# Optimization experiments

Measured on AMD Instinct MI355X. Metric: run time of the kernel, lower is better.

## Reference

```python
import jax, jax.numpy as jnp
import numpy as np

R = 32  # voxel resolution
B, CIN, COUT, N = 4, 64, 64, 4096
K = 3


def setup_inputs():
    key = jax.random.key(0)
    ks = jax.random.split(key, 8)
    s = 0.05
    return {
        "features": jax.random.normal(ks[0], (B, CIN, N), jnp.float32),
        "coords": jax.random.normal(ks[1], (B, 3, N), jnp.float32),
        # voxel branch: conv3d + BN x2
        "w1": jax.random.normal(ks[2], (COUT, CIN, K, K, K), jnp.float32) * s,
        "b1": jnp.zeros((COUT,), jnp.float32),
        "g1": jnp.ones((COUT,), jnp.float32),
        "be1": jnp.zeros((COUT,), jnp.float32),
        "w2": jax.random.normal(ks[3], (COUT, COUT, K, K, K), jnp.float32) * s,
        "b2": jnp.zeros((COUT,), jnp.float32),
        "g2": jnp.ones((COUT,), jnp.float32),
        "be2": jnp.zeros((COUT,), jnp.float32),
        # point branch SharedMLP (1x1 conv + BN + ReLU)
        "wp": jax.random.normal(ks[4], (COUT, CIN), jnp.float32) * s,
        "bp": jnp.zeros((COUT,), jnp.float32),
        "gp": jnp.ones((COUT,), jnp.float32),
        "bep": jnp.zeros((COUT,), jnp.float32),
        # fuzzy_proj 1x1 conv
        "wf": jax.random.normal(ks[5], (COUT, CIN), jnp.float32) * s,
        "bf": jnp.zeros((COUT,), jnp.float32),
        # fusion SharedMLP (3*COUT -> COUT)
        "wfu": jax.random.normal(ks[6], (COUT, 3 * COUT), jnp.float32) * s,
        "bfu": jnp.zeros((COUT,), jnp.float32),
        "gfu": jnp.ones((COUT,), jnp.float32),
        "befu": jnp.zeros((COUT,), jnp.float32),
    }


def _bn3d(x, g, b):
    # training-mode BatchNorm3d, eps=1e-4 (biased variance, as torch)
    m = x.mean((0, 2, 3, 4), keepdims=True)
    v = x.var((0, 2, 3, 4), keepdims=True)
    return (x - m) * jax.lax.rsqrt(v + 1e-4) * g[None, :, None, None, None] + b[None, :, None, None, None]


def _bn1d(x, g, b):
    m = x.mean((0, 2), keepdims=True)
    v = x.var((0, 2), keepdims=True)
    return (x - m) * jax.lax.rsqrt(v + 1e-4) * g[None, :, None] + b[None, :, None]


def _conv3d(x, w, b):
    pad = K // 2
    y = jax.lax.conv_general_dilated(x, w, (1, 1, 1), [(pad, pad)] * 3,
                                     dimension_numbers=('NCDHW', 'OIDHW', 'NCDHW'))
    return y + b[None, :, None, None, None]


def _conv1x1(x, w, b):
    return jnp.einsum('oc,bcn->bon', w, x) + b[None, :, None]


def _voxelize(features, coords):
    # PVCNN Voxelization(normalize=True, eps=0): center, scale to unit, grid coords in [0, R-1]
    nc = coords - coords.mean(axis=2, keepdims=True)              # [B,3,N]
    norm = jnp.linalg.norm(nc, axis=1, keepdims=True)             # [B,1,N]
    nc = nc / (norm.max(axis=2, keepdims=True) * 2.0) + 0.5
    nc = jnp.clip(nc * R, 0.0, R - 1)
    vox = jnp.round(nc).astype(jnp.int32)                         # [B,3,N]
    b_, c_, n_ = features.shape
    idx = (vox[:, 0] * R + vox[:, 1]) * R + vox[:, 2]             # [B,N]
    flat = (idx + jnp.arange(b_)[:, None] * R ** 3).reshape(-1)
    feat = features.transpose(0, 2, 1).reshape(b_ * n_, c_)
    sums = jax.ops.segment_sum(feat, flat, num_segments=b_ * R ** 3)
    cnt = jax.ops.segment_sum(jnp.ones((b_ * n_,), feat.dtype), flat, num_segments=b_ * R ** 3)
    avg = sums / jnp.maximum(cnt, 1.0)[:, None]                   # scatter-mean
    grid = avg.reshape(b_, R ** 3, c_).transpose(0, 2, 1).reshape(b_, c_, R, R, R)
    return grid, nc


def _devoxelize(grid, nc):
    # trilinear gather: grid [B,C,R,R,R], nc [B,3,N] float coords in [0,R-1]
    b_, c_ = grid.shape[:2]
    g = grid.reshape(b_, c_, -1)
    lo_f = jnp.floor(nc)
    fr = nc - lo_f                                                # fractional part [B,3,N]
    lo = lo_f.astype(jnp.int32)
    hi = jnp.minimum(lo + 1, R - 1)
    out = jnp.zeros((b_, c_, nc.shape[2]), grid.dtype)
    for dx in (0, 1):
        for dy in (0, 1):
            for dz in (0, 1):
                ix = hi[:, 0] if dx else lo[:, 0]
                iy = hi[:, 1] if dy else lo[:, 1]
                iz = hi[:, 2] if dz else lo[:, 2]
                w = ((fr[:, 0] if dx else 1.0 - fr[:, 0]) *
                     (fr[:, 1] if dy else 1.0 - fr[:, 1]) *
                     (fr[:, 2] if dz else 1.0 - fr[:, 2]))        # [B,N]
                flat = (ix * R + iy) * R + iz                     # [B,N]
                vals = jnp.take_along_axis(g, flat[:, None, :], axis=2)  # [B,C,N]
                out = out + vals * w[:, None, :]
    return out


def reference(features, coords, w1, b1, g1, be1, w2, b2, g2, be2,
              wp, bp, gp, bep, wf, bf, wfu, bfu, gfu, befu):
    lrelu = lambda x: jnp.where(x > 0, x, 0.1 * x)
    # voxel branch
    grid, nc = _voxelize(features, coords)
    v = lrelu(_bn3d(_conv3d(grid, w1, b1), g1, be1))
    v = lrelu(_bn3d(_conv3d(v, w2, b2), g2, be2))
    vox_feat = _devoxelize(v, nc)                                 # [B,COUT,N]
    # point branch
    pt = jax.nn.relu(_bn1d(_conv1x1(features, wp, bp), gp, bep))
    # fuzzy branch: dense attention over points
    cn = coords.transpose(0, 2, 1)                                # [B,N,3]
    cn = cn / jnp.maximum(jnp.linalg.norm(cn, axis=-1, keepdims=True), 1e-12)
    att = jax.nn.softmax(jnp.einsum('bnd,bmd->bnm', cn, cn) / 0.1, axis=-1)
    fz = jnp.einsum('bnm,bcm->bcn', att, features)                # [B,CIN,N]
    fz = _conv1x1(fz, wf, bf)
    # fusion
    comb = jnp.concatenate([vox_feat, pt, fz], axis=1)            # [B,3*COUT,N]
    fused = jax.nn.relu(_bn1d(_conv1x1(comb, wfu, bfu), gfu, befu))
    return (fused, coords)
```

## Files before the change

### kernel.cpp

```cpp
#include <hip/hip_runtime.h>
#include <hip/hip_bf16.h>
#include <math.h>

#define RR 32
#define R3 32768
#define BB 4
#define CI 64
#define CO 64
#define NN 4096

typedef short v8s __attribute__((ext_vector_type(8)));
typedef float v4f __attribute__((ext_vector_type(4)));
typedef unsigned short ushort_t;

__device__ __forceinline__ unsigned short f2bf(float f) {
    unsigned int u = __float_as_uint(f);
    unsigned int r = (u + 0x7FFFu + ((u >> 16) & 1u)) >> 16;
    return (unsigned short)r;
}

__device__ __forceinline__ void gll16(const void* g, void* l) {
    __builtin_amdgcn_global_load_lds((const __attribute__((address_space(1))) unsigned int*)g,
                                     (__attribute__((address_space(3))) unsigned int*)l, 16, 0, 0);
}

__device__ __forceinline__ float blockReduceSum(float v, float* sm) {
    int tid = threadIdx.x;
    sm[tid] = v; __syncthreads();
    for (int off = 128; off > 0; off >>= 1) {
        if (tid < off) sm[tid] += sm[tid + off];
        __syncthreads();
    }
    float r = sm[0]; __syncthreads();
    return r;
}
__device__ __forceinline__ float blockReduceMax(float v, float* sm) {
    int tid = threadIdx.x;
    sm[tid] = v; __syncthreads();
    for (int off = 128; off > 0; off >>= 1) {
        if (tid < off) sm[tid] = fmaxf(sm[tid], sm[tid + off]);
        __syncthreads();
    }
    float r = sm[0]; __syncthreads();
    return r;
}

__global__ void k_nc(const float* __restrict__ coords, float* __restrict__ nc,
                     int* __restrict__ vidx, int* __restrict__ cntI) {
    int b = blockIdx.x, tid = threadIdx.x;
    __shared__ float sm[256];
    const float* cb = coords + (size_t)b * 3 * NN;
    float s0 = 0, s1 = 0, s2 = 0;
    for (int n = tid; n < NN; n += 256) {
        s0 += cb[n]; s1 += cb[NN + n]; s2 += cb[2 * NN + n];
    }
    float m0 = blockReduceSum(s0, sm) * (1.0f / NN);
    float m1 = blockReduceSum(s1, sm) * (1.0f / NN);
    float m2 = blockReduceSum(s2, sm) * (1.0f / NN);
    float mx = 0;
    for (int n = tid; n < NN; n += 256) {
        float dx = cb[n] - m0, dy = cb[NN + n] - m1, dz = cb[2 * NN + n] - m2;
        mx = fmaxf(mx, dx * dx + dy * dy + dz * dz);
    }
    mx = blockReduceMax(mx, sm);
    float denom = 2.0f * sqrtf(mx);
    float mean[3] = {m0, m1, m2};
    for (int n = tid; n < NN; n += 256) {
        int vi[3];
        #pragma unroll
        for (int ax = 0; ax < 3; ax++) {
            float x = (cb[ax * NN + n] - mean[ax]) / denom + 0.5f;
            x = x * RR;
            x = fminf(fmaxf(x, 0.0f), (float)(RR - 1));
            nc[((size_t)b * 3 + ax) * NN + n] = x;
            vi[ax] = (int)rintf(x);
        }
        int idx = (vi[0] * RR + vi[1]) * RR + vi[2];
        vidx[b * NN + n] = idx;
        atomicAdd(&cntI[b * R3 + idx], 1);
    }
}

__global__ void k_scan1(const int* __restrict__ cntI, int* __restrict__ lscan,
                        int* __restrict__ bsum) {
    __shared__ int sm[256];
    int tid = threadIdx.x;
    int i = blockIdx.x * 256 + tid;
    int v = cntI[i];
    sm[tid] = v; __syncthreads();
    for (int off = 1; off < 256; off <<= 1) {
        int t = (tid >= off) ? sm[tid - off] : 0;
        __syncthreads();
        sm[tid] += t;
        __syncthreads();
    }
    lscan[i] = sm[tid] - v;
    if (tid == 255) bsum[blockIdx.x] = sm[tid];
}

__global__ void k_scan2(const int* __restrict__ bsum, int* __restrict__ bbase) {
    __shared__ int sm[512];
    int tid = threadIdx.x;
    int v = bsum[tid];
    sm[tid] = v; __syncthreads();
    for (int off = 1; off < 512; off <<= 1) {
        int t = (tid >= off) ? sm[tid - off] : 0;
        __syncthreads();
        sm[tid] += t;
        __syncthreads();
    }
    bbase[tid] = sm[tid] - v;
}

__global__ void k_fill(const int* __restrict__ vidx, const int* __restrict__ lscan,
                       const int* __restrict__ bbase, int* __restrict__ rank,
                       int* __restrict__ plist) {
    int i = blockIdx.x * 256 + threadIdx.x;
    int b = i >> 12, n = i & (NN - 1);
    int flat = b * R3 + vidx[i];
    int r = atomicAdd(&rank[flat], 1);
    plist[bbase[flat >> 8] + lscan[flat] + r] = n;
}

__global__ void k_tfcl(const float* __restrict__ feat, float* __restrict__ featT) {
    __shared__ float t[64][65];
    int b = blockIdx.y, n0 = blockIdx.x * 64, tid = threadIdx.x;
    int q = tid >> 6, nl = tid & 63;
    #pragma unroll
    for (int k = 0; k < 16; k++) {
        int c = q * 16 + k;
        t[nl][c] = feat[((size_t)(b * CI + c)) * NN + n0 + nl];
    }
    __syncthreads();
    #pragma unroll
    for (int k = 0; k < 16; k++) {
        int n = q * 16 + k;
        featT[((size_t)b * NN + n0 + n) * 64 + nl] = t[n][nl];
    }
}

__global__ __launch_bounds__(256) void k_gather(const float* __restrict__ featT,
                                                const int* __restrict__ cntI,
                                                const int* __restrict__ lscan,
                                                const int* __restrict__ bbase,
                                                const int* __restrict__ plist,
                                                ushort_t* __restrict__ gT) {
    int wv = threadIdx.x >> 6, lane = threadIdx.x & 63;
    int vbase = blockIdx.x * 32 + wv * 8;
    for (int k = 0; k < 8; k++) {
        int flat = vbase + k;
        int count = cntI[flat];
        float s = 0.0f;
        if (count > 0) {
            int b = flat >> 15;
            int start = bbase[flat >> 8] + lscan[flat];
            for (int j = 0; j < count; j++) {
                int n = plist[start + j];
                s += featT[((size_t)b * NN + n) * 64 + lane];
            }
            s *= 1.0f / (float)count;
        }
        gT[(size_t)flat * 64 + lane] = f2bf(s);
    }
}

__global__ void k_f2b(const float* __restrict__ x, ushort_t* __restrict__ o) {
    size_t i = (size_t)blockIdx.x * 256 + threadIdx.x;
    float4 a = ((const float4*)x)[i * 2];
    float4 b = ((const float4*)x)[i * 2 + 1];
    union { __hip_bfloat162 h[4]; uint4 u; } pk;
    pk.h[0] = __float22bfloat162_rn(make_float2(a.x, a.y));
    pk.h[1] = __float22bfloat162_rn(make_float2(a.z, a.w));
    pk.h[2] = __float22bfloat162_rn(make_float2(b.x, b.y));
    pk.h[3] = __float22bfloat162_rn(make_float2(b.z, b.w));
    ((uint4*)o)[i] = pk.u;
}

__global__ void k_tws(const float* __restrict__ w, ushort_t* __restrict__ wS) {
    int i = blockIdx.x * 256 + threadIdx.x;
    int cis = i & 31, co = (i >> 5) & 63;
    int dx = (i >> 11) % 3, cih = (i / 6144) & 1, dzdy = i / 12288;
    int k = dzdy * 3 + dx, ci = cih * 32 + cis;
    wS[i] = f2bf(w[((size_t)co * CI + ci) * 27 + k]);
}

__global__ void k_fold(const float* __restrict__ wp, const float* __restrict__ wfu,
                       const float* __restrict__ wf, const float* __restrict__ bf,
                       const float* __restrict__ bfu,
                       float* __restrict__ wpT, float* __restrict__ wfuT,
                       float* __restrict__ bC) {
    int i = blockIdx.x * 256 + threadIdx.x;
    if (i < 4096) {
        int c = i >> 6, o = i & 63;
        wpT[c * 64 + o] = wp[o * 64 + c];
    } else if (i < 12288) {
        int j = i - 4096;
        int c = j >> 6, o = j & 63;
        wfuT[c * 64 + o] = wfu[(size_t)o * 192 + c];
    } else if (i < 16384) {
        int j = i - 12288;
        int c = j >> 6, o = j & 63;
        float s = 0;
        for (int k = 0; k < 64; k++)
            s += wfu[(size_t)o * 192 + 128 + k] * wf[(size_t)k * 64 + c];
        wfuT[(128 + c) * 64 + o] = s;
    } else if (i < 16448) {
        int o = i - 16384;
        float s = bfu[o];
        for (int k = 0; k < 64; k++)
            s += wfu[(size_t)o * 192 + 128 + k] * bf[k];
        bC[o] = s;
    }
}

__global__ void k_bncast(const float* __restrict__ x, const float* __restrict__ accs,
                         const float* __restrict__ g, const float* __restrict__ be,
                         float invcnt, float slope, ushort_t* __restrict__ o) {
    size_t i = (size_t)blockIdx.x * 256 + threadIdx.x;
    int c0 = (int)((i * 8) & 63);
    float sc[8], sh[8];
    #pragma unroll
    for (int j = 0; j < 8; j++) {
        int c = c0 + j;
        float mean = accs[2 * c] * invcnt;
        float var = accs[2 * c + 1] * invcnt - mean * mean;
        float scale = g[c] * rsqrtf(var + 1e-4f);
        sc[j] = scale;
        sh[j] = be[c] - mean * scale;
    }
    float4 a = ((const float4*)x)[i * 2];
    float4 d = ((const float4*)x)[i * 2 + 1];
    float va[8] = {a.x, a.y, a.z, a.w, d.x, d.y, d.z, d.w};
    unsigned pk[4];
    #pragma unroll
    for (int j = 0; j < 4; j++) {
        float u0 = va[2 * j] * sc[2 * j] + sh[2 * j];
        float u1 = va[2 * j + 1] * sc[2 * j + 1] + sh[2 * j + 1];
        u0 = u0 > 0 ? u0 : slope * u0;
        u1 = u1 > 0 ? u1 : slope * u1;
        pk[j] = (unsigned)f2bf(u0) | ((unsigned)f2bf(u1) << 16);
    }
    ((uint4*)o)[i] = make_uint4(pk[0], pk[1], pk[2], pk[3]);
}

__global__ __launch_bounds__(256) void k_convlds(const ushort_t* __restrict__ gT,
                                                 const ushort_t* __restrict__ wS,
                                                 float* __restrict__ outCL,
                                                 float* __restrict__ accs) {
    __shared__ ushort_t lin[20480];
    __shared__ ushort_t lw[2][6144];
    int bid = blockIdx.x;
    int wgid = (bid & 7) * 64 + (bid >> 3);
    int yt = wgid & 3, z0 = (wgid >> 2) & 31, b = wgid >> 7;
    int tid = threadIdx.x;
    int w = __builtin_amdgcn_readfirstlane(tid >> 6);
    int lane = tid & 63, l15 = lane & 15, l4 = lane >> 4;
    int y0 = yt * 8;
    const ushort_t* gTb = gT + (size_t)b * R3 * 64;

    int voxF[4];
    #pragma unroll
    for (int f = 0; f < 4; f++)
        voxF[f] = (w * 2 + (f >> 1)) * 32 + (f & 1) * 16 + l15 - 1;
    bool xlo_ok = (l15 != 0), xhi_ok = (l15 != 15);

    const v8s vzero = {};
    v4f acc[4][4];
    #pragma unroll
    for (int m = 0; m < 4; m++)
        #pragma unroll
        for (int f = 0; f < 4; f++)
            acc[m][f] = (v4f){0.0f, 0.0f, 0.0f, 0.0f};

#define WSTAGE(s)                                                              \
    do {                                                                       \
        const ushort_t* _src = wS + (size_t)(s) * 6144;                        \
        ushort_t* _dst = lw[(s) & 1];                                          \
        _Pragma("unroll") for (int _i = 0; _i < 3; _i++) {                     \
            int _p = _i * 256 + w * 64;                                        \
            gll16(_src + (size_t)(_p + lane) * 8, _dst + (size_t)_p * 8);      \
        }                                                                      \
    } while (0)

#define ISTAGE(dz)                                                             \
    do {                                                                       \
        int _zp = z0 - 1 + (dz);                                               \
        if (_zp < 0 || _zp > 31) {                                             \
            for (int _q = 0; _q < 10; _q++)                                    \
                *(v8s*)&lin[(size_t)(w * 640 + _q * 64 + lane) * 8] = vzero;   \
        } else {                                                               \
            if (yt == 0) *(v8s*)&lin[(size_t)tid * 8] = vzero;                 \
            if (yt == 3) *(v8s*)&lin[(size_t)(2304 + tid) * 8] = vzero;        \
            const ushort_t* _pb = gTb + ((size_t)_zp * 1024 + (size_t)(y0 - 1) * 32) * 64; \
            int _g0 = (yt == 0) ? 256 : 0;                                     \
            int _nc = 10 - (yt == 0) - (yt == 3);                              \
            for (int _i = 0; _i < _nc; _i++) {                                 \
                int _pbase = _g0 + _i * 256 + w * 64;                          \
                int _p = _pbase + lane;                                        \
                int _vx = _p >> 3, _js = _p & 7;                               \
                int _sg = _vx * 8 + (_js ^ (_vx & 7));                         \
                gll16(_pb + (size_t)_sg * 8, lin + (size_t)_pbase * 8);        \
            }                                                                  \
        }                                                                      \
    } while (0)

    WSTAGE(0);
    for (int s = 0; s < 18; s++) {
        int dy = (s / 2) % 3, cih = s & 1;
        asm volatile("s_barrier" ::: "memory");
        if ((s % 6) == 0) ISTAGE(s / 6);
        if (s + 1 < 18) WSTAGE(s + 1);
        if (s + 1 < 18) asm volatile("s_waitcnt vmcnt(3) lgkmcnt(0)" ::: "memory");
        else            asm volatile("s_waitcnt vmcnt(0) lgkmcnt(0)" ::: "memory");
        asm volatile("s_barrier" ::: "memory");

        const ushort_t* lwb = lw[s & 1];
        #pragma unroll
        for (int dx = 0; dx < 3; dx++) {
            v8s Bf[4];
            #pragma unroll
            for (int f = 0; f < 4; f++) {
                int vox = voxF[f] + dy * 32 + dx;
                int g = vox * 8 + ((cih * 4 + l4) ^ (vox & 7));
                int bix = g * 16;
                bix = bix < 0 ? 0 : bix;
                v8s vb = *(const v8s*)((const char*)lin + bix);
                bool ok = (dx == 0 && (f & 1) == 0) ? xlo_ok :
                          (dx == 2 && (f & 1) == 1) ? xhi_ok : true;
                Bf[f] = ok ? vb : vzero;
            }
            const ushort_t* ap = lwb + dx * 2048 + l15 * 32 + l4 * 8;
            #pragma unroll
            for (int m = 0; m < 4; m++) {
                v8s Af = *(const v8s*)(ap + m * 512);
                #pragma unroll
                for (int f = 0; f < 4; f++)
                    acc[m][f] = __builtin_amdgcn_mfma_f32_16x16x32_bf16(Af, Bf[f], acc[m][f], 0, 0, 0);
            }
        }
    }

    #pragma unroll
    for (int m = 0; m < 4; m++) {
        #pragma unroll
        for (int f = 0; f < 4; f++) {
            int y = y0 + w * 2 + (f >> 1);
            int x = (f & 1) * 16 + l15;
            float4 o = make_float4(acc[m][f][0], acc[m][f][1], acc[m][f][2], acc[m][f][3]);
            *(float4*)&outCL[((size_t)b * R3 + z0 * 1024 + y * 32 + x) * 64 + m * 16 + l4 * 4] = o;
        }
    }

    __syncthreads();
    float* sbuf = (float*)lin;
    #pragma unroll
    for (int m = 0; m < 4; m++)
        #pragma unroll
        for (int r = 0; r < 4; r++) {
            float s = 0, q = 0;
            #pragma unroll
            for (int f = 0; f < 4; f++) {
                float v = acc[m][f][r];
                s += v; q += v * v;
            }
            sbuf[tid * 32 + (m * 4 + r) * 2] = s;
            sbuf[tid * 32 + (m * 4 + r) * 2 + 1] = q;
        }
    __syncthreads();
    if (tid < 128) {
        int co = tid >> 1, val = tid & 1;
        int m = co >> 4, cl4 = (co >> 2) & 3, r = co & 3;
        float a = 0;
        for (int w2 = 0; w2 < 4; w2++)
            for (int l = 0; l < 16; l++)
                a += sbuf[(w2 * 64 + cl4 * 16 + l) * 32 + (m * 4 + r) * 2 + val];
        atomicAdd(&accs[2 * co + val], a);
    }
#undef WSTAGE
#undef ISTAGE
}

__global__ void k_bnfin2(const float* __restrict__ pst, const float* __restrict__ g,
                         const float* __restrict__ be, float* __restrict__ stats,
                         float invcnt) {
    int c = blockIdx.x, tid = threadIdx.x;
    __shared__ float rs[256], rq[256];
    rs[tid] = pst[(c * 256 + tid) * 2];
    rq[tid] = pst[(c * 256 + tid) * 2 + 1];
    __syncthreads();
    for (int off = 128; off > 0; off >>= 1) {
        if (tid < off) { rs[tid] += rs[tid + off]; rq[tid] += rq[tid + off]; }
        __syncthreads();
    }
    if (tid == 0) {
        float mean = rs[0] * invcnt;
        float var = rq[0] * invcnt - mean * mean;
        float sc = g[c] * rsqrtf(var + 1e-4f);
        stats[2 * c] = sc;
        stats[2 * c + 1] = be[c] - mean * sc;
    }
}

__global__ void k_bn_act(const float* __restrict__ x, const float* __restrict__ stats,
                         float* __restrict__ out, int shift, float slope) {
    size_t i = (size_t)blockIdx.x * 256 + threadIdx.x;
    int c = (int)((i >> shift) & 63);
    float sc = stats[2 * c], sh = stats[2 * c + 1];
    float4 v = ((const float4*)x)[i];
    v.x = v.x * sc + sh; v.y = v.y * sc + sh; v.z = v.z * sc + sh; v.w = v.w * sc + sh;
    v.x = v.x > 0 ? v.x : slope * v.x;
    v.y = v.y > 0 ? v.y : slope * v.y;
    v.z = v.z > 0 ? v.z : slope * v.z;
    v.w = v.w > 0 ? v.w : slope * v.w;
    ((float4*)out)[i] = v;
}

__global__ void k_devox2(const float* __restrict__ gcl, const float* __restrict__ accs,
                         const float* __restrict__ g, const float* __restrict__ be,
                         float invcnt, const float* __restrict__ nc,
                         float* __restrict__ out) {
    int b = blockIdx.y;
    int tid = threadIdx.x, p = tid >> 4, q = tid & 15;
    int n = blockIdx.x * 16 + p;
    float x = nc[((size_t)b * 3 + 0) * NN + n];
    float y = nc[((size_t)b * 3 + 1) * NN + n];
    float z = nc[((size_t)b * 3 + 2) * NN + n];
    float fx = floorf(x), fy = floorf(y), fz = floorf(z);
    int lx = (int)fx, ly = (int)fy, lz = (int)fz;
    int hx = min(lx + 1, RR - 1), hy = min(ly + 1, RR - 1), hz = min(lz + 1, RR - 1);
    float frx = x - fx, fry = y - fy, frz = z - fz;
    int xx[2] = {lx, hx}, yy[2] = {ly, hy}, zz[2] = {lz, hz};
    float wx[2] = {1.0f - frx, frx}, wy[2] = {1.0f - fry, fry}, wz[2] = {1.0f - frz, frz};
    float sc[4], sh[4];
    #pragma unroll
    for (int j = 0; j < 4; j++) {
        int c = q * 4 + j;
        float mean = accs[2 * c] * invcnt;
        float var = accs[2 * c + 1] * invcnt - mean * mean;
        float scale = g[c] * rsqrtf(var + 1e-4f);
        sc[j] = scale;
        sh[j] = be[c] - mean * scale;
    }
    float a0 = 0, a1 = 0, a2 = 0, a3 = 0;
    #pragma unroll
    for (int dx = 0; dx < 2; dx++)
        #pragma unroll
        for (int dy = 0; dy < 2; dy++)
            #pragma unroll
            for (int dz = 0; dz < 2; dz++) {
                int idx = (xx[dx] * RR + yy[dy]) * RR + zz[dz];
                float wt = wx[dx] * wy[dy] * wz[dz];
                float4 v = *(const float4*)&gcl[((size_t)b * R3 + idx) * 64 + q * 4];
                float u0 = v.x * sc[0] + sh[0]; u0 = u0 > 0 ? u0 : 0.1f * u0;
                float u1 = v.y * sc[1] + sh[1]; u1 = u1 > 0 ? u1 : 0.1f * u1;
                float u2 = v.z * sc[2] + sh[2]; u2 = u2 > 0 ? u2 : 0.1f * u2;
                float u3 = v.w * sc[3] + sh[3]; u3 = u3 > 0 ? u3 : 0.1f * u3;
                a0 += wt * u0; a1 += wt * u1; a2 += wt * u2; a3 += wt * u3;
            }
    out[((size_t)(b * 64 + q * 4 + 0)) * NN + n] = a0;
    out[((size_t)(b * 64 + q * 4 + 1)) * NN + n] = a1;
    out[((size_t)(b * 64 + q * 4 + 2)) * NN + n] = a2;
    out[((size_t)(b * 64 + q * 4 + 3)) * NN + n] = a3;
}

__global__ __launch_bounds__(256) void k_fuzzym(const float* __restrict__ coords,
                                                const ushort_t* __restrict__ featb,
                                                float* __restrict__ pnum,
                                                float* __restrict__ pden) {
    __shared__ float cm[3][1024];
    __shared__ ushort_t la[2][2048];
    int b = blockIdx.z, mc = blockIdx.y, nt = blockIdx.x;
    int tid = threadIdx.x;
    int w = tid >> 6, lane = tid & 63, l15 = lane & 15, l4 = lane >> 4;
    int m0 = mc * 1024;

    for (int i = tid; i < 1024; i += 256) {
        float a0 = coords[((size_t)b * 3 + 0) * NN + m0 + i];
        float a1 = coords[((size_t)b * 3 + 1) * NN + m0 + i];
        float a2 = coords[((size_t)b * 3 + 2) * NN + m0 + i];
        float inv = 1.0f / fmaxf(sqrtf(a0 * a0 + a1 * a1 + a2 * a2), 1e-12f);
        cm[0][i] = a0 * inv; cm[1][i] = a1 * inv; cm[2][i] = a2 * inv;
    }

    int n = nt * 64 + w * 16 + l15;
    float q0 = coords[((size_t)b * 3 + 0) * NN + n];
    float q1 = coords[((size_t)b * 3 + 1) * NN + n];
    float q2 = coords[((size_t)b * 3 + 2) * NN + n];
    float qi = 10.0f / fmaxf(sqrtf(q0 * q0 + q1 * q1 + q2 * q2), 1e-12f);
    q0 *= qi; q1 *= qi; q2 *= qi;

    int srow = tid >> 2, sslot = tid & 3;
    int g0 = sslot ^ ((srow >> 1) & 3);
    const ushort_t* fb = featb + (size_t)b * 64 * NN + m0;
    const ushort_t* sbase = fb + (size_t)srow * NN + g0 * 8;
    int rsw = (l15 >> 1) & 3;

    v4f acc[4];
    #pragma unroll
    for (int cb = 0; cb < 4; cb++) acc[cb] = (v4f){0.0f, 0.0f, 0.0f, 0.0f};
    float den = 0.0f;

    gll16(sbase, &la[0][(size_t)tid * 8]);
    asm volatile("s_waitcnt vmcnt(0)" ::: "memory");
    __syncthreads();

    for (int t = 0; t < 32; t++) {
        int cur = t & 1;
        if (t + 1 < 32)
            gll16(sbase + (t + 1) * 32, &la[cur ^ 1][(size_t)tid * 8]);

        int mo = t * 32 + l4 * 8;
        float e[8];
        #pragma unroll
        for (int jj = 0; jj < 2; jj++) {
            float4 x0 = *(const float4*)&cm[0][mo + jj * 4];
            float4 x1 = *(const float4*)&cm[1][mo + jj * 4];
            float4 x2 = *(const float4*)&cm[2][mo + jj * 4];
            e[jj * 4 + 0] = __expf(q0 * x0.x + q1 * x1.x + q2 * x2.x);
            e[jj * 4 + 1] = __expf(q0 * x0.y + q1 * x1.y + q2 * x2.y);
            e[jj * 4 + 2] = __expf(q0 * x0.z + q1 * x1.z + q2 * x2.z);
            e[jj * 4 + 3] = __expf(q0 * x0.w + q1 * x1.w + q2 * x2.w);
        }
        den += ((e[0] + e[1]) + (e[2] + e[3])) + ((e[4] + e[5]) + (e[6] + e[7]));
        union { __hip_bfloat162 h[4]; v8s v; } pk;
        pk.h[0] = __float22bfloat162_rn(make_float2(e[0], e[1]));
        pk.h[1] = __float22bfloat162_rn(make_float2(e[2], e[3]));
        pk.h[2] = __float22bfloat162_rn(make_float2(e[4], e[5]));
        pk.h[3] = __float22bfloat162_rn(make_float2(e[6], e[7]));
        #pragma unroll
        for (int cb = 0; cb < 4; cb++) {
            v8s A = *(const v8s*)&la[cur][(size_t)((cb * 16 + l15) * 4 + (l4 ^ rsw)) * 8];
            acc[cb] = __builtin_amdgcn_mfma_f32_16x16x32_bf16(A, pk.v, acc[cb], 0, 0, 0);
        }
        asm volatile("s_waitcnt vmcnt(0)" ::: "memory");
        __syncthreads();
    }

    den += __shfl_xor(den, 16);
    den += __shfl_xor(den, 32);

    size_t obase = ((size_t)(b * 4 + mc)) * 64 * NN;
    #pragma unroll
    for (int cb = 0; cb < 4; cb++)
        #pragma unroll
        for (int r = 0; r < 4; r++)
            pnum[obase + (size_t)(cb * 16 + l4 * 4 + r) * NN + n] = acc[cb][r];
    if (l4 == 0) pden[((size_t)(b * 4 + mc)) * NN + n] = den;
}

__global__ void k_combine2(const float* __restrict__ pnum, const float* __restrict__ pden,
                           float* __restrict__ fzf) {
    int i = blockIdx.x * 256 + threadIdx.x;
    int b = i >> 18, c = (i >> 12) & 63, n = i & 4095;
    float num = 0, den = 0;
    #pragma unroll
    for (int ch = 0; ch < 4; ch++) {
        num += pnum[((size_t)(b * 4 + ch) * 64 + c) * NN + n];
        den += pden[((size_t)(b * 4 + ch)) * NN + n];
    }
    fzf[((size_t)(b * 64 + c)) * NN + n] = num / den;
}

__global__ __launch_bounds__(256) void k_1x1s(const float* __restrict__ in,
                                              const float* __restrict__ wT,
                                              const float* __restrict__ bias,
                                              float* __restrict__ out,
                                              float* __restrict__ pst) {
    int b = blockIdx.z, ob = blockIdx.y, bx = blockIdx.x;
    int tid = threadIdx.x;
    int q = tid & 15, o = ob * 16 + (tid >> 4);
    int n = bx * 64 + q * 4;
    const float* src = in + (size_t)b * 64 * NN + n;
    const float* wp_ = wT + o;
    v4f acc = {0, 0, 0, 0};
    #pragma unroll 8
    for (int c = 0; c < 64; c++) {
        float4 x = *(const float4*)&src[(size_t)c * NN];
        float w = wp_[c * 64];
        acc[0] += x.x * w; acc[1] += x.y * w; acc[2] += x.z * w; acc[3] += x.w * w;
    }
    float bv = bias[o];
    float s = 0, q2 = 0;
    float4 ov;
    float* op = (float*)&ov;
    #pragma unroll
    for (int v = 0; v < 4; v++) {
        float val = acc[v] + bv;
        op[v] = val;
        s += val; q2 += val * val;
    }
    *(float4*)&out[((size_t)(b * 64 + o)) * NN + n] = ov;
    #pragma unroll
    for (int off = 1; off < 16; off <<= 1) {
        s += __shfl_xor(s, off);
        q2 += __shfl_xor(q2, off);
    }
    if (q == 0) {
        int part = bx * 4 + b;
        pst[(o * 256 + part) * 2] = s;
        pst[(o * 256 + part) * 2 + 1] = q2;
    }
}

__global__ __launch_bounds__(256) void k_1x1f(const float* __restrict__ vox,
                                              const float* __restrict__ pt,
                                              const float* __restrict__ fzf,
                                              const float* __restrict__ bnB,
                                              const float* __restrict__ wfuT,
                                              const float* __restrict__ bC,
                                              float* __restrict__ out,
                                              float* __restrict__ pst) {
    int b = blockIdx.z, ob = blockIdx.y, bx = blockIdx.x;
    int tid = threadIdx.x;
    int q = tid & 15, o = ob * 16 + (tid >> 4);
    int n = bx * 64 + q * 4;
    const float* srcA = vox + (size_t)b * 64 * NN + n;
    const float* srcB = pt + (size_t)b * 64 * NN + n;
    const float* srcC = fzf + (size_t)b * 64 * NN + n;
    const float* wA = wfuT + o;
    v4f acc = {0, 0, 0, 0};
    #pragma unroll 8
    for (int c = 0; c < 64; c++) {
        float4 x = *(const float4*)&srcA[(size_t)c * NN];
        float w = wA[c * 64];
        acc[0] += x.x * w; acc[1] += x.y * w; acc[2] += x.z * w; acc[3] += x.w * w;
    }
    #pragma unroll 8
    for (int c = 0; c < 64; c++) {
        float4 x = *(const float4*)&srcB[(size_t)c * NN];
        float sc = bnB[2 * c], sh = bnB[2 * c + 1];
        float w = wA[(64 + c) * 64];
        float x0 = fmaxf(x.x * sc + sh, 0.0f), x1 = fmaxf(x.y * sc + sh, 0.0f);
        float x2 = fmaxf(x.z * sc + sh, 0.0f), x3 = fmaxf(x.w * sc + sh, 0.0f);
        acc[0] += x0 * w; acc[1] += x1 * w; acc[2] += x2 * w; acc[3] += x3 * w;
    }
    #pragma unroll 8
    for (int c = 0; c < 64; c++) {
        float4 x = *(const float4*)&srcC[(size_t)c * NN];
        float w = wA[(128 + c) * 64];
        acc[0] += x.x * w; acc[1] += x.y * w; acc[2] += x.z * w; acc[3] += x.w * w;
    }
    float bv = bC[o];
    float s = 0, q2 = 0;
    float4 ov;
    float* op = (float*)&ov;
    #pragma unroll
    for (int v = 0; v < 4; v++) {
        float val = acc[v] + bv;
        op[v] = val;
        s += val; q2 += val * val;
    }
    *(float4*)&out[((size_t)(b * 64 + o)) * NN + n] = ov;
    #pragma unroll
    for (int off = 1; off < 16; off <<= 1) {
        s += __shfl_xor(s, off);
        q2 += __shfl_xor(q2, off);
    }
    if (q == 0) {
        int part = bx * 4 + b;
        pst[(o * 256 + part) * 2] = s;
        pst[(o * 256 + part) * 2 + 1] = q2;
    }
}

extern "C" void kernel_launch(void* const* d_in, const int* in_sizes, int n_in,
                              void* d_out, int out_size, void* d_ws, size_t ws_size,
                              hipStream_t stream) {
    const float* features = (const float*)d_in[0];
    const float* coords = (const float*)d_in[1];
    const float* w1 = (const float*)d_in[2];
    const float* g1 = (const float*)d_in[4];
    const float* be1 = (const float*)d_in[5];
    const float* w2 = (const float*)d_in[6];
    const float* g2 = (const float*)d_in[8];
    const float* be2 = (const float*)d_in[9];
    const float* wp = (const float*)d_in[10];
    const float* bp = (const float*)d_in[11];
    const float* gp = (const float*)d_in[12];
    const float* bep = (const float*)d_in[13];
    const float* wf = (const float*)d_in[14];
    const float* bf = (const float*)d_in[15];
    const float* wfu = (const float*)d_in[16];
    const float* bfu = (const float*)d_in[17];
    const float* gfu = (const float*)d_in[18];
    const float* befu = (const float*)d_in[19];

    float* ws = (float*)d_ws;
    float* nc = ws;
    int* vidx = (int*)(ws + 49152);
    int* cntI = (int*)(ws + 65536);
    float* pden = ws + 65536;
    float* gridCL = ws + 196608;
    int* lscan = (int*)(ws + 196608);
    int* bsum = (int*)(ws + 327680);
    int* bbase = (int*)(ws + 328192);
    int* rank = (int*)(ws + 328704);
    int* plist = (int*)(ws + 459776);
    float* featT = ws + 476160;
    float* gTpool = ws + 8585216;
    ushort_t* gT = (ushort_t*)gTpool;
    float* pnum = gTpool;
    float* pstB = gTpool;
    float* stats = ws + 16973824;
    float* voxreg = ws + 16974336;
    ushort_t* wS1 = (ushort_t*)voxreg;
    ushort_t* wS2 = wS1 + 110592;
    float* vox = voxreg;
    float* pt = ws + 18022912;
    float* fzf = ws + 19071488;
    float* wpT = ws + 20120064;
    float* wfuT = wpT + 4096;
    float* bC = wfuT + 12288;
    float* fpre = ws + 21168640;
    ushort_t* featb = (ushort_t*)fpre;
    float* accs = ws + 22217216;

    float* out = (float*)d_out;

    hipMemsetAsync(accs, 0, 512 * 4, stream);
    hipMemsetAsync(cntI, 0, 131072 * 4, stream);
    hipMemsetAsync(rank, 0, 131072 * 4, stream);

    k_fold<<<65, 256, 0, stream>>>(wp, wfu, wf, bf, bfu, wpT, wfuT, bC);
    k_f2b<<<BB * 64 * NN / 8 / 256, 256, 0, stream>>>(features, featb);
    k_tws<<<432, 256, 0, stream>>>(w1, wS1);
    k_tws<<<432, 256, 0, stream>>>(w2, wS2);
    k_tfcl<<<dim3(64, BB), 256, 0, stream>>>(features, featT);

    k_nc<<<BB, 256, 0, stream>>>(coords, nc, vidx, cntI);
    k_scan1<<<512, 256, 0, stream>>>(cntI, lscan, bsum);
    k_scan2<<<1, 512, 0, stream>>>(bsum, bbase);
    k_fill<<<BB * NN / 256, 256, 0, stream>>>(vidx, lscan, bbase, rank, plist);
    k_gather<<<4096, 256, 0, stream>>>(featT, cntI, lscan, bbase, plist, gT);

    k_convlds<<<512, 256, 0, stream>>>(gT, wS1, gridCL, accs);
    k_bncast<<<BB * R3 * 64 / 8 / 256, 256, 0, stream>>>(gridCL, accs, g1, be1,
                                                         1.0f / (BB * R3), 0.1f, gT);
    k_convlds<<<512, 256, 0, stream>>>(gT, wS2, gridCL, accs + 128);
    k_devox2<<<dim3(NN / 16, BB), 256, 0, stream>>>(gridCL, accs + 128, g2, be2,
                                                    1.0f / (BB * R3), nc, vox);

    k_fuzzym<<<dim3(64, 4, BB), 256, 0, stream>>>(coords, featb, pnum, pden);
    k_combine2<<<BB * 64 * NN / 256, 256, 0, stream>>>(pnum, pden, fzf);

    k_1x1s<<<dim3(NN / 64, 4, BB), 256, 0, stream>>>(features, wpT, bp, pt, pstB);
    k_bnfin2<<<64, 256, 0, stream>>>(pstB, gp, bep, stats + 256, 1.0f / (BB * NN));

    k_1x1f<<<dim3(NN / 64, 4, BB), 256, 0, stream>>>(vox, pt, fzf, stats + 256, wfuT, bC,
                                                     fpre, pstB);
    k_bnfin2<<<64, 256, 0, stream>>>(pstB, gfu, befu, stats + 384, 1.0f / (BB * NN));
    k_bn_act<<<BB * 64 * NN / 4 / 256, 256, 0, stream>>>(fpre, stats + 384, out, 10, 0.0f);

    hipMemcpyAsync(out + (size_t)BB * CO * NN, coords, (size_t)BB * 3 * NN * 4,
                   hipMemcpyDeviceToDevice, stream);
}
```

Before: 275.1 us.

## Store first conv output as bf16 and single-buffer conv weight staging

```diff
diff --git a/kernel.cpp b/kernel.cpp
--- a/kernel.cpp
+++ b/kernel.cpp
@@ -17,6 +17,9 @@
     unsigned int u = __float_as_uint(f);
     unsigned int r = (u + 0x7FFFu + ((u >> 16) & 1u)) >> 16;
     return (unsigned short)r;
+}
+__device__ __forceinline__ float bf2f(unsigned short h) {
+    return __uint_as_float((unsigned int)h << 16);
 }
 
 __device__ __forceinline__ void gll16(const void* g, void* l) {
@@ -213,9 +216,9 @@
     }
 }
 
-__global__ void k_bncast(const float* __restrict__ x, const float* __restrict__ accs,
-                         const float* __restrict__ g, const float* __restrict__ be,
-                         float invcnt, float slope, ushort_t* __restrict__ o) {
+__global__ void k_bncast2(const ushort_t* __restrict__ x, const float* __restrict__ accs,
+                          const float* __restrict__ g, const float* __restrict__ be,
+                          float invcnt, float slope, ushort_t* __restrict__ o) {
     size_t i = (size_t)blockIdx.x * 256 + threadIdx.x;
     int c0 = (int)((i * 8) & 63);
     float sc[8], sh[8];
@@ -228,14 +231,13 @@
         sc[j] = scale;
         sh[j] = be[c] - mean * scale;
     }
-    float4 a = ((const float4*)x)[i * 2];
-    float4 d = ((const float4*)x)[i * 2 + 1];
-    float va[8] = {a.x, a.y, a.z, a.w, d.x, d.y, d.z, d.w};
+    uint4 in = ((const uint4*)x)[i];
+    unsigned iv[4] = {in.x, in.y, in.z, in.w};
     unsigned pk[4];
     #pragma unroll
     for (int j = 0; j < 4; j++) {
-        float u0 = va[2 * j] * sc[2 * j] + sh[2 * j];
-        float u1 = va[2 * j + 1] * sc[2 * j + 1] + sh[2 * j + 1];
+        float u0 = bf2f((unsigned short)(iv[j] & 0xFFFF)) * sc[2 * j] + sh[2 * j];
+        float u1 = bf2f((unsigned short)(iv[j] >> 16)) * sc[2 * j + 1] + sh[2 * j + 1];
         u0 = u0 > 0 ? u0 : slope * u0;
         u1 = u1 > 0 ? u1 : slope * u1;
         pk[j] = (unsigned)f2bf(u0) | ((unsigned)f2bf(u1) << 16);
@@ -243,12 +245,13 @@
     ((uint4*)o)[i] = make_uint4(pk[0], pk[1], pk[2], pk[3]);
 }
 
+template <int OUTBF16>
 __global__ __launch_bounds__(256) void k_convlds(const ushort_t* __restrict__ gT,
                                                  const ushort_t* __restrict__ wS,
-                                                 float* __restrict__ outCL,
+                                                 void* __restrict__ outP,
                                                  float* __restrict__ accs) {
     __shared__ ushort_t lin[20480];
-    __shared__ ushort_t lw[2][6144];
+    __shared__ ushort_t lw[6144];
     int bid = blockIdx.x;
     int wgid = (bid & 7) * 64 + (bid >> 3);
     int yt = wgid & 3, z0 = (wgid >> 2) & 31, b = wgid >> 7;
@@ -275,10 +278,9 @@
 #define WSTAGE(s)                                                              \
     do {                                                                       \
         const ushort_t* _src = wS + (size_t)(s) * 6144;                        \
-        ushort_t* _dst = lw[(s) & 1];                                          \
         _Pragma("unroll") for (int _i = 0; _i < 3; _i++) {                     \
             int _p = _i * 256 + w * 64;                                        \
-            gll16(_src + (size_t)(_p + lane) * 8, _dst + (size_t)_p * 8);      \
+            gll16(_src + (size_t)(_p + lane) * 8, lw + (size_t)_p * 8);        \
         }                                                                      \
     } while (0)
 
@@ -304,17 +306,14 @@
         }                                                                      \
     } while (0)
 
-    WSTAGE(0);
     for (int s = 0; s < 18; s++) {
         int dy = (s / 2) % 3, cih = s & 1;
         asm volatile("s_barrier" ::: "memory");
         if ((s % 6) == 0) ISTAGE(s / 6);
-        if (s + 1 < 18) WSTAGE(s + 1);
-        if (s + 1 < 18) asm volatile("s_waitcnt vmcnt(3) lgkmcnt(0)" ::: "memory");
-        else            asm volatile("s_waitcnt vmcnt(0) lgkmcnt(0)" ::: "memory");
+        WSTAGE(s);
+        asm volatile("s_waitcnt vmcnt(0) lgkmcnt(0)" ::: "memory");
         asm volatile("s_barrier" ::: "memory");
 
-        const ushort_t* lwb = lw[s & 1];
         #pragma unroll
         for (int dx = 0; dx < 3; dx++) {
             v8s Bf[4];
@@ -329,7 +328,7 @@
                           (dx == 2 && (f & 1) == 1) ? xhi_ok : true;
                 Bf[f] = ok ? vb : vzero;
             }
-            const ushort_t* ap = lwb + dx * 2048 + l15 * 32 + l4 * 8;
+            const ushort_t* ap = lw + dx * 2048 + l15 * 32 + l4 * 8;
             #pragma unroll
             for (int m = 0; m < 4; m++) {
                 v8s Af = *(const v8s*)(ap + m * 512);
@@ -346,8 +345,15 @@
         for (int f = 0; f < 4; f++) {
             int y = y0 + w * 2 + (f >> 1);
             int x = (f & 1) * 16 + l15;
-            float4 o = make_float4(acc[m][f][0], acc[m][f][1], acc[m][f][2], acc[m][f][3]);
-            *(float4*)&outCL[((size_t)b * R3 + z0 * 1024 + y * 32 + x) * 64 + m * 16 + l4 * 4] = o;
+            size_t base = ((size_t)b * R3 + z0 * 1024 + y * 32 + x) * 64 + m * 16 + l4 * 4;
+            if (OUTBF16) {
+                unsigned p0 = (unsigned)f2bf(acc[m][f][0]) | ((unsigned)f2bf(acc[m][f][1]) << 16);
+                unsigned p1 = (unsigned)f2bf(acc[m][f][2]) | ((unsigned)f2bf(acc[m][f][3]) << 16);
+                *(uint2*)&((ushort_t*)outP)[base] = make_uint2(p0, p1);
+            } else {
+                float4 o = make_float4(acc[m][f][0], acc[m][f][1], acc[m][f][2], acc[m][f][3]);
+                *(float4*)&((float*)outP)[base] = o;
+            }
         }
     }
 
@@ -691,6 +697,7 @@
     int* cntI = (int*)(ws + 65536);
     float* pden = ws + 65536;
     float* gridCL = ws + 196608;
+    ushort_t* gTraw = (ushort_t*)gridCL;
     int* lscan = (int*)(ws + 196608);
     int* bsum = (int*)(ws + 327680);
     int* bbase = (int*)(ws + 328192);
@@ -733,10 +740,10 @@
     k_fill<<<BB * NN / 256, 256, 0, stream>>>(vidx, lscan, bbase, rank, plist);
     k_gather<<<4096, 256, 0, stream>>>(featT, cntI, lscan, bbase, plist, gT);
 
-    k_convlds<<<512, 256, 0, stream>>>(gT, wS1, gridCL, accs);
-    k_bncast<<<BB * R3 * 64 / 8 / 256, 256, 0, stream>>>(gridCL, accs, g1, be1,
-                                                         1.0f / (BB * R3), 0.1f, gT);
-    k_convlds<<<512, 256, 0, stream>>>(gT, wS2, gridCL, accs + 128);
+    k_convlds<1><<<512, 256, 0, stream>>>(gT, wS1, gTraw, accs);
+    k_bncast2<<<BB * R3 * 64 / 8 / 256, 256, 0, stream>>>(gTraw, accs, g1, be1,
+                                                          1.0f / (BB * R3), 0.1f, gT);
+    k_convlds<0><<<512, 256, 0, stream>>>(gT, wS2, gridCL, accs + 128);
     k_devox2<<<dim3(NN / 16, BB), 256, 0, stream>>>(gridCL, accs + 128, g2, be2,
                                                     1.0f / (BB * R3), nc, vox);
 
```

After: 278.8 us. About the same (+1.3%).
